# Optimization experiments

Measured on AMD Instinct MI355X. Metric: run time of the kernel, lower is better.

Reference implementation:

```python
import jax, jax.numpy as jnp
import numpy as np

K = 3  # kernel_size
P = K * K  # patch length per channel


def setup_inputs() -> dict:
    key = jax.random.key(0)
    k1, k2 = jax.random.split(key)
    B, H, W, C_in, C_out = 16, 64, 64, 64, 64
    L = P * (P + 1) // 2 + P + 1  # 45 quadratic + 9 linear + 1 bias = 55
    x = jax.random.normal(k1, (B, H, W, C_in), dtype=jnp.float32)
    # glorot-ish scale for the flat kernel [1,1,L,C_in,C_out]
    flat_kernel = jax.random.normal(k2, (1, 1, L, C_in, C_out), dtype=jnp.float32) * 0.05
    return {"x": x, "flat_kernel": flat_kernel}


def _quadratic_features(x):
    # x: [B,H,W,C] NHWC; stride 1, 'same' padding, k=3
    B, H, W, C = x.shape
    pad = K // 2
    xp = jnp.pad(x, ((0, 0), (pad, pad), (pad, pad), (0, 0)))
    # patches: [B,H,W,P,C] -- loop is over the 9 fixed kernel taps only
    patches = jnp.stack(
        [xp[:, i:i + H, j:j + W, :] for i in range(K) for j in range(K)], axis=3
    )
    iu, ju = np.triu_indices(P)  # all pairs i<=j incl. squares -> 45 terms
    quad = patches[:, :, :, iu, :] * patches[:, :, :, ju, :]  # [B,H,W,45,C]
    ones = jnp.ones_like(patches[:, :, :, :1, :])              # bias term
    # flat features per the use_linear_and_bias=True layout: [quad | linear | 1]
    return jnp.concatenate([quad, patches, ones], axis=3)       # [B,H,W,55,C]


def reference(x, flat_kernel):
    feats = _quadratic_features(x)          # [B,H,W,L,C]
    w = flat_kernel[0, 0]                   # [L,C,O]
    # contract over flat-feature index L and input channels C
    return jnp.einsum('bhwlc,lco->bhwo', feats, w)
```

## Files before the change

kernel.cpp:

```cpp
#include <hip/hip_runtime.h>

typedef _Float16 half8 __attribute__((ext_vector_type(8)));
typedef _Float16 half4v __attribute__((ext_vector_type(4)));
typedef float f32x16 __attribute__((ext_vector_type(16)));

#define BOFF 0
#define XOFF 55296
#define LDS_TOTAL 80640

__device__ __forceinline__ void stage16(const void* g, const void* l) {
  __builtin_amdgcn_global_load_lds(
      (const __attribute__((address_space(1))) unsigned int*)(unsigned long long)g,
      (__attribute__((address_space(3))) unsigned int*)(unsigned int)(unsigned long long)l,
      16, 0, 0);
}

__global__ __launch_bounds__(256)
void prepack_kernel(const float* __restrict__ W, _Float16* __restrict__ Bp) {
  const int idx = blockIdx.x * 256 + threadIdx.x;
  if (idx < 221184) {
    const int v   = idx & 7;
    const int lam = (idx >> 3) & 63;
    const int f   = idx >> 9;
    const int l   = f % 54;
    const int r   = f / 54;
    const int cc  = r & 1;
    const int ks  = (r >> 1) & 1;
    const int nt  = (r >> 2) & 1;
    const int c   = (ks * 2 + cc) * 16 + (lam >> 5) * 8 + v;
    const int o   = nt * 32 + (lam & 31);
    Bp[idx] = (_Float16)W[(l * 64 + c) * 64 + o];
  } else if (idx < 221184 + 64) {
    const int o = idx - 221184;
    float s = 0.f;
    for (int c = 0; c < 64; ++c) s += W[(54 * 64 + c) * 64 + o];
    ((float*)(Bp + 221184))[o] = s;
  }
}

__global__ __launch_bounds__(256, 2)
void qconv_kernel(const float* __restrict__ x, const _Float16* __restrict__ Bp,
                  float* __restrict__ out) {
  constexpr int IU[45] = {0,0,0,0,0,0,0,0,0, 1,1,1,1,1,1,1,1, 2,2,2,2,2,2,2,
                          3,3,3,3,3,3, 4,4,4,4,4, 5,5,5,5, 6,6,6, 7,7, 8};
  constexpr int JU[45] = {0,1,2,3,4,5,6,7,8, 1,2,3,4,5,6,7,8, 2,3,4,5,6,7,8,
                          3,4,5,6,7,8, 4,5,6,7,8, 5,6,7,8, 6,7,8, 7,8, 8};

  const int tid  = threadIdx.x;
  const int wave = tid >> 6;
  const int lane = tid & 63;
  const int colA = lane & 31;
  const int kg   = lane >> 5;

  const int phys = blockIdx.x;
  const int logical = (phys & 7) * 64 + (phys >> 3);
  const int nt  = logical & 1;
  const int grp = logical >> 1;
  const int b   = grp >> 4;
  const int r0  = (grp & 15) * 4;
  const int r   = r0 + wave;

  __shared__ __align__(16) unsigned char smem[LDS_TOTAL];
  const char* BpB = (const char*)Bp;

  f32x16 acc[2] = {};
  half8 tap[2][9];
  half8 bqE[6], bqO[6];

#define LOADQ(buf, p)                                                       \
  _Pragma("unroll")                                                         \
  for (int q = 0; q < 6; ++q)                                               \
    buf[q] = *(const half8*)(smem + BOFF + ((p) * 6 + q) * 1024 + lane * 16);

#define WAITSB(n)                                                           \
  asm volatile("s_waitcnt lgkmcnt(" #n ")" ::: "memory");                   \
  __builtin_amdgcn_sched_barrier(0);

#define MFMA6(buf, l0)                                                      \
  __builtin_amdgcn_s_setprio(1);                                            \
  _Pragma("unroll")                                                         \
  for (int q = 0; q < 6; ++q) {                                             \
    const int l = (l0) + q;                                                 \
    half8 a0, a1;                                                           \
    if (l < 45) { a0 = tap[0][IU[l]] * tap[0][JU[l]];                       \
                  a1 = tap[1][IU[l]] * tap[1][JU[l]]; }                     \
    else        { a0 = tap[0][l - 45]; a1 = tap[1][l - 45]; }               \
    acc[0] = __builtin_amdgcn_mfma_f32_32x32x16_f16(a0, buf[q], acc[0],     \
                                                    0, 0, 0);               \
    acc[1] = __builtin_amdgcn_mfma_f32_32x32x16_f16(a1, buf[q], acc[1],     \
                                                    0, 0, 0);               \
  }                                                                         \
  __builtin_amdgcn_s_setprio(0);

  for (int p = 0; p < 4; ++p) {
    const int ks = p >> 1;
    const int cc = p & 1;
    __syncthreads();

    const size_t bsrc = (size_t)(((nt * 2 + ks) * 2 + cc) * 54) * 1024;
    for (int f = wave; f < 54; f += 4)
      stage16(BpB + bsrc + (size_t)f * 1024 + lane * 16,
              (char*)smem + BOFF + f * 1024);

    if (cc == 0) {
      for (int idx = tid; idx < 3168; idx += 256) {
        const int row = idx / 528;
        const int rem = idx - row * 528;
        const int col = rem >> 3;
        const int gq  = rem & 7;
        const int hh  = r0 - 1 + row;
        const int ww  = col - 1;
        float4 v = make_float4(0.f, 0.f, 0.f, 0.f);
        if ((unsigned)hh < 64u && (unsigned)ww < 64u)
          v = *(const float4*)(x + ((((size_t)b * 64 + hh) * 64 + ww) * 64
                                    + ks * 32 + gq * 4));
        half4v hv;
        hv[0] = (_Float16)v.x; hv[1] = (_Float16)v.y;
        hv[2] = (_Float16)v.z; hv[3] = (_Float16)v.w;
        const int addr = XOFF + ((row * 4224 + col * 64 + gq * 8)
                                 ^ (((col >> 1) & 3) << 4));
        *(half4v*)(smem + addr) = hv;
      }
    }

    asm volatile("s_waitcnt vmcnt(0)" ::: "memory");
    __syncthreads();

#pragma unroll
    for (int mt = 0; mt < 2; ++mt)
#pragma unroll
      for (int t = 0; t < 9; ++t) {
        const int xrow = wave + t / 3;
        const int ce   = mt * 32 + colA + (t % 3);
        const int aa = XOFF + ((xrow * 4224 + ce * 64 + cc * 32 + kg * 16)
                               ^ (((ce >> 1) & 3) << 4));
        tap[mt][t] = *(const half8*)(smem + aa);
      }

    LOADQ(bqE, 0);
    LOADQ(bqO, 1);  WAITSB(6);  MFMA6(bqE, 0);
    LOADQ(bqE, 2);  WAITSB(6);  MFMA6(bqO, 6);
    LOADQ(bqO, 3);  WAITSB(6);  MFMA6(bqE, 12);
    LOADQ(bqE, 4);  WAITSB(6);  MFMA6(bqO, 18);
    LOADQ(bqO, 5);  WAITSB(6);  MFMA6(bqE, 24);
    LOADQ(bqE, 6);  WAITSB(6);  MFMA6(bqO, 30);
    LOADQ(bqO, 7);  WAITSB(6);  MFMA6(bqE, 36);
    LOADQ(bqE, 8);  WAITSB(6);  MFMA6(bqO, 42);
                    WAITSB(0);  MFMA6(bqE, 48);
  }

  const float bias = ((const float*)(BpB + 442368))[nt * 32 + colA];
#pragma unroll
  for (int mt = 0; mt < 2; ++mt) {
    float* op = out + (((size_t)b * 64 + r) * 64 + mt * 32) * 64
                    + nt * 32 + colA;
#pragma unroll
    for (int gi = 0; gi < 16; ++gi) {
      const int rowD = (gi & 3) + 8 * (gi >> 2) + 4 * kg;
      op[(size_t)rowD * 64] = acc[mt][gi] + bias;
    }
  }
}

extern "C" void kernel_launch(void* const* d_in, const int* in_sizes, int n_in,
                              void* d_out, int out_size, void* d_ws, size_t ws_size,
                              hipStream_t stream) {
  const float* x = (const float*)d_in[0];
  const float* W = (const float*)d_in[1];
  float* out     = (float*)d_out;
  _Float16* Bp   = (_Float16*)d_ws;

  prepack_kernel<<<dim3((221248 + 255) / 256), dim3(256), 0, stream>>>(W, Bp);
  qconv_kernel<<<dim3(512), dim3(256), 0, stream>>>(x, Bp, out);
}
```

Baseline: 42.26 us.

## Prepack input to padded fp16 layout and double-buffer weight staging in LDS

Adds a separate kernel that converts x to fp16 in a channel-group-major, column-padded layout, so the conv kernel loads taps straight from global memory into registers instead of staging x through LDS. The weight staging is split into half-phases that are double-buffered across two LDS slots, so the next slice of weights loads asynchronously while MFMAs run on the current one. LDS use drops, which may allow more resident blocks. In exchange there is an extra kernel launch and a full fp16 copy of x written to and read back from global memory, and taps are now read from global memory with row-boundary predication.

```diff
diff --git a/kernel.cpp b/kernel.cpp
--- a/kernel.cpp
+++ b/kernel.cpp
@@ -1,12 +1,11 @@
 #include <hip/hip_runtime.h>
 
 typedef _Float16 half8 __attribute__((ext_vector_type(8)));
-typedef _Float16 half4v __attribute__((ext_vector_type(4)));
 typedef float f32x16 __attribute__((ext_vector_type(16)));
 
-#define BOFF 0
-#define XOFF 55296
-#define LDS_TOTAL 80640
+#define SLOT 27648
+#define LDS_TOTAL (2 * SLOT)
+#define PX_OFF 450560
 
 __device__ __forceinline__ void stage16(const void* g, const void* l) {
   __builtin_amdgcn_global_load_lds(
@@ -24,10 +23,9 @@
     const int f   = idx >> 9;
     const int l   = f % 54;
     const int r   = f / 54;
-    const int cc  = r & 1;
-    const int ks  = (r >> 1) & 1;
-    const int nt  = (r >> 2) & 1;
-    const int c   = (ks * 2 + cc) * 16 + (lam >> 5) * 8 + v;
+    const int set = r & 3;
+    const int nt  = r >> 2;
+    const int c   = set * 16 + (lam >> 5) * 8 + v;
     const int o   = nt * 32 + (lam & 31);
     Bp[idx] = (_Float16)W[(l * 64 + c) * 64 + o];
   } else if (idx < 221184 + 64) {
@@ -38,9 +36,33 @@
   }
 }
 
+__global__ __launch_bounds__(256)
+void xpack_kernel(const float* __restrict__ x, _Float16* __restrict__ px) {
+  const int idx = blockIdx.x * 256 + threadIdx.x;
+  if (idx >= 16 * 64 * 64 * 8) return;
+  const int ch8 = idx & 7;
+  const int col = (idx >> 3) & 63;
+  const int row = (idx >> 9) & 63;
+  const int b   = idx >> 15;
+  const float* src = x + ((((size_t)b * 64 + row) * 64 + col) * 64) + ch8 * 8;
+  const float4 v0 = *(const float4*)src;
+  const float4 v1 = *(const float4*)(src + 4);
+  half8 h;
+  h[0] = (_Float16)v0.x; h[1] = (_Float16)v0.y;
+  h[2] = (_Float16)v0.z; h[3] = (_Float16)v0.w;
+  h[4] = (_Float16)v1.x; h[5] = (_Float16)v1.y;
+  h[6] = (_Float16)v1.z; h[7] = (_Float16)v1.w;
+  const size_t base = (((size_t)b * 8 + ch8) * 64 + row) * 66;
+  *(half8*)(px + (base + col + 1) * 8) = h;
+  if (col == 0) {
+    half8 z = {};
+    *(half8*)(px + (base + 0) * 8)  = z;
+    *(half8*)(px + (base + 65) * 8) = z;
+  }
+}
+
 __global__ __launch_bounds__(256, 2)
-void qconv_kernel(const float* __restrict__ x, const _Float16* __restrict__ Bp,
-                  float* __restrict__ out) {
+void qconv_kernel(const _Float16* __restrict__ Bp, float* __restrict__ out) {
   constexpr int IU[45] = {0,0,0,0,0,0,0,0,0, 1,1,1,1,1,1,1,1, 2,2,2,2,2,2,2,
                           3,3,3,3,3,3, 4,4,4,4,4, 5,5,5,5, 6,6,6, 7,7, 8};
   constexpr int JU[45] = {0,1,2,3,4,5,6,7,8, 1,2,3,4,5,6,7,8, 2,3,4,5,6,7,8,
@@ -62,91 +84,86 @@
 
   __shared__ __align__(16) unsigned char smem[LDS_TOTAL];
   const char* BpB = (const char*)Bp;
+  const _Float16* px = (const _Float16*)(BpB + PX_OFF);
 
   f32x16 acc[2] = {};
-  half8 tap[2][9];
-  half8 bqE[6], bqO[6];
+  half8 tapA[2][9], tapB[2][9];
+  half8 bqE[9], bqO[9];
 
-#define LOADQ(buf, p)                                                       \
+#define TAPG(TP, SET)                                                       \
   _Pragma("unroll")                                                         \
-  for (int q = 0; q < 6; ++q)                                               \
-    buf[q] = *(const half8*)(smem + BOFF + ((p) * 6 + q) * 1024 + lane * 16);
+  for (int t = 0; t < 9; ++t) {                                             \
+    const int rr = r + t / 3 - 1;                                           \
+    const bool ok = ((unsigned)rr < 64u);                                   \
+    _Pragma("unroll")                                                       \
+    for (int mt = 0; mt < 2; ++mt) {                                        \
+      half8 tv = {};                                                        \
+      if (ok)                                                               \
+        tv = *(const half8*)(px + ((((size_t)b * 8 + (SET) * 2 + kg) * 64   \
+              + rr) * 66 + (mt * 32 + colA + t % 3)) * 8);                  \
+      TP[mt][t] = tv;                                                       \
+    }                                                                       \
+  }
+
+#define LOADQ9(BUFQ, BUF, PH)                                               \
+  _Pragma("unroll")                                                         \
+  for (int q = 0; q < 9; ++q)                                               \
+    BUFQ[q] = *(const half8*)(smem + (BUF) * SLOT + ((PH) * 9 + q) * 1024   \
+                              + lane * 16);
 
 #define WAITSB(n)                                                           \
   asm volatile("s_waitcnt lgkmcnt(" #n ")" ::: "memory");                   \
   __builtin_amdgcn_sched_barrier(0);
 
-#define MFMA6(buf, l0)                                                      \
+#define MFMA9(TP, BUFQ, L0)                                                 \
   __builtin_amdgcn_s_setprio(1);                                            \
   _Pragma("unroll")                                                         \
-  for (int q = 0; q < 6; ++q) {                                             \
-    const int l = (l0) + q;                                                 \
+  for (int q = 0; q < 9; ++q) {                                             \
+    const int l = (L0) + q;                                                 \
     half8 a0, a1;                                                           \
-    if (l < 45) { a0 = tap[0][IU[l]] * tap[0][JU[l]];                       \
-                  a1 = tap[1][IU[l]] * tap[1][JU[l]]; }                     \
-    else        { a0 = tap[0][l - 45]; a1 = tap[1][l - 45]; }               \
-    acc[0] = __builtin_amdgcn_mfma_f32_32x32x16_f16(a0, buf[q], acc[0],     \
+    if (l < 45) { a0 = TP[0][IU[l]] * TP[0][JU[l]];                         \
+                  a1 = TP[1][IU[l]] * TP[1][JU[l]]; }                       \
+    else        { a0 = TP[0][l - 45]; a1 = TP[1][l - 45]; }                 \
+    acc[0] = __builtin_amdgcn_mfma_f32_32x32x16_f16(a0, BUFQ[q], acc[0],    \
                                                     0, 0, 0);               \
-    acc[1] = __builtin_amdgcn_mfma_f32_32x32x16_f16(a1, buf[q], acc[1],     \
+    acc[1] = __builtin_amdgcn_mfma_f32_32x32x16_f16(a1, BUFQ[q], acc[1],    \
                                                     0, 0, 0);               \
   }                                                                         \
   __builtin_amdgcn_s_setprio(0);
 
-  for (int p = 0; p < 4; ++p) {
-    const int ks = p >> 1;
-    const int cc = p & 1;
-    __syncthreads();
+#define ROUND(BUF, NBUF, LH, TP, DOSTG, SBN, LHN)                           \
+  {                                                                         \
+    if (DOSTG)                                                              \
+      for (int f = wave; f < 27; f += 4)                                    \
+        stage16(BpB + (SBN) + (size_t)((LHN) * 27 + f) * 1024 + lane * 16,  \
+                (char*)smem + (NBUF) * SLOT + f * 1024);                    \
+    LOADQ9(bqE, BUF, 0);                                                    \
+    LOADQ9(bqO, BUF, 1);  WAITSB(9);  MFMA9(TP, bqE, (LH) * 27 + 0);        \
+    LOADQ9(bqE, BUF, 2);  WAITSB(9);  MFMA9(TP, bqO, (LH) * 27 + 9);        \
+                          WAITSB(0);  MFMA9(TP, bqE, (LH) * 27 + 18);       \
+    asm volatile("s_waitcnt vmcnt(0)" ::: "memory");                        \
+    __syncthreads();                                                        \
+  }
 
-    const size_t bsrc = (size_t)(((nt * 2 + ks) * 2 + cc) * 54) * 1024;
-    for (int f = wave; f < 54; f += 4)
-      stage16(BpB + bsrc + (size_t)f * 1024 + lane * 16,
-              (char*)smem + BOFF + f * 1024);
-
-    if (cc == 0) {
-      for (int idx = tid; idx < 3168; idx += 256) {
-        const int row = idx / 528;
-        const int rem = idx - row * 528;
-        const int col = rem >> 3;
-        const int gq  = rem & 7;
-        const int hh  = r0 - 1 + row;
-        const int ww  = col - 1;
-        float4 v = make_float4(0.f, 0.f, 0.f, 0.f);
-        if ((unsigned)hh < 64u && (unsigned)ww < 64u)
-          v = *(const float4*)(x + ((((size_t)b * 64 + hh) * 64 + ww) * 64
-                                    + ks * 32 + gq * 4));
-        half4v hv;
-        hv[0] = (_Float16)v.x; hv[1] = (_Float16)v.y;
-        hv[2] = (_Float16)v.z; hv[3] = (_Float16)v.w;
-        const int addr = XOFF + ((row * 4224 + col * 64 + gq * 8)
-                                 ^ (((col >> 1) & 3) << 4));
-        *(half4v*)(smem + addr) = hv;
-      }
-    }
-
+  {
+    const size_t sb = (size_t)(nt * 4) * 55296;
+    for (int f = wave; f < 27; f += 4)
+      stage16(BpB + sb + (size_t)f * 1024 + lane * 16,
+              (char*)smem + f * 1024);
     asm volatile("s_waitcnt vmcnt(0)" ::: "memory");
     __syncthreads();
+  }
 
-#pragma unroll
-    for (int mt = 0; mt < 2; ++mt)
-#pragma unroll
-      for (int t = 0; t < 9; ++t) {
-        const int xrow = wave + t / 3;
-        const int ce   = mt * 32 + colA + (t % 3);
-        const int aa = XOFF + ((xrow * 4224 + ce * 64 + cc * 32 + kg * 16)
-                               ^ (((ce >> 1) & 3) << 4));
-        tap[mt][t] = *(const half8*)(smem + aa);
-      }
-
-    LOADQ(bqE, 0);
-    LOADQ(bqO, 1);  WAITSB(6);  MFMA6(bqE, 0);
-    LOADQ(bqE, 2);  WAITSB(6);  MFMA6(bqO, 6);
-    LOADQ(bqO, 3);  WAITSB(6);  MFMA6(bqE, 12);
-    LOADQ(bqE, 4);  WAITSB(6);  MFMA6(bqO, 18);
-    LOADQ(bqO, 5);  WAITSB(6);  MFMA6(bqE, 24);
-    LOADQ(bqE, 6);  WAITSB(6);  MFMA6(bqO, 30);
-    LOADQ(bqO, 7);  WAITSB(6);  MFMA6(bqE, 36);
-    LOADQ(bqE, 8);  WAITSB(6);  MFMA6(bqO, 42);
-                    WAITSB(0);  MFMA6(bqE, 48);
+  for (int su = 0; su < 2; ++su) {
+    const size_t sb0 = (size_t)(nt * 4 + su * 2) * 55296;
+    const size_t sb1 = sb0 + 55296;
+    const size_t sb2 = sb1 + 55296;
+    TAPG(tapA, su * 2);
+    ROUND(0, 1, 0, tapA, 1,         sb0, 1);
+    ROUND(1, 0, 1, tapA, 1,         sb1, 0);
+    TAPG(tapB, su * 2 + 1);
+    ROUND(0, 1, 0, tapB, 1,         sb1, 1);
+    ROUND(1, 0, 1, tapB, (su == 0), sb2, 0);
   }
 
   const float bias = ((const float*)(BpB + 442368))[nt * 32 + colA];
@@ -169,7 +186,9 @@
   const float* W = (const float*)d_in[1];
   float* out     = (float*)d_out;
   _Float16* Bp   = (_Float16*)d_ws;
+  _Float16* px   = (_Float16*)((char*)d_ws + PX_OFF);
 
   prepack_kernel<<<dim3((221248 + 255) / 256), dim3(256), 0, stream>>>(W, Bp);
-  qconv_kernel<<<dim3(512), dim3(256), 0, stream>>>(x, Bp, out);
+  xpack_kernel<<<dim3(2048), dim3(256), 0, stream>>>(x, px);
+  qconv_kernel<<<dim3(512), dim3(256), 0, stream>>>(Bp, out);
 }
```

Measured after the change: 48.75 us. 1.15x slower.
